# Optimization experiments

Measured on AMD Instinct MI355X. Metric: run time of the kernel, lower is better.

The kernel has to match this reference:

```python
import jax, jax.numpy as jnp
import numpy as np

N_HEADS = 16
HEAD_DIM = 64
STRIDE = 32  # default local_attention_ctx used as stride in 'strided' mode


def _strided_fill_mask(n):
    # Faithful to the torch code: positions where (i >= j) and ((i - j) % stride == 0)
    # get mask value 1, and the code does masked_fill_(mask == 1, -inf),
    # i.e. those positions are set to -inf (inverted polarity, replicated as-is).
    i = jnp.arange(n)[:, None]
    j = jnp.arange(n)[None, :]
    return (i >= j) & (((i - j) % STRIDE) == 0)  # [n, n] bool, True -> -inf


def setup_inputs() -> dict:
    key = jax.random.key(0)
    k_x, k_qkv, k_out = jax.random.split(key, 3)
    b, n, c = 2, 2048, 1024
    inner = N_HEADS * HEAD_DIM  # 1024
    x = jax.random.normal(k_x, (b, n, c), dtype=jnp.float32)
    W_qkv = jax.random.normal(k_qkv, (c, 3 * inner), dtype=jnp.float32) * 0.02
    W_out = jax.random.normal(k_out, (inner, c), dtype=jnp.float32) * 0.02
    b_out = jnp.zeros((c,), dtype=jnp.float32)
    return {"x": x, "W_qkv": W_qkv, "W_out": W_out, "b_out": b_out}


def reference(x, W_qkv, W_out, b_out):
    b, n, c = x.shape
    h, hd = N_HEADS, HEAD_DIM
    scale = c ** (-0.5)  # n_embeddings ** -0.5, as in the original

    qkv = x @ W_qkv                              # [b, n, 3*h*hd]
    q, k, v = jnp.split(qkv, 3, axis=-1)
    def to_heads(t):
        return t.reshape(b, n, h, hd).transpose(0, 2, 1, 3)  # [b, h, n, hd]
    q, k, v = to_heads(q), to_heads(k), to_heads(v)

    dots = jnp.einsum('bhid,bhjd->bhij', q, k) * scale       # [b, h, n, n]
    fill = _strided_fill_mask(n)                             # [n, n]
    dots = jnp.where(fill[None, None], -jnp.inf, dots)

    attn = jax.nn.softmax(dots, axis=-1)
    out = jnp.einsum('bhij,bhjd->bhid', attn, v)             # [b, h, n, hd]
    out = out.transpose(0, 2, 1, 3).reshape(b, n, h * hd)    # [b, n, inner]
    out = out @ W_out + b_out                                # dropout: eval/identity
    return out
```

## Files before the change

kernel.cpp:

```cpp
#include <hip/hip_runtime.h>

typedef __attribute__((ext_vector_type(8))) short bf16x8;
typedef __attribute__((ext_vector_type(4))) float f32x4;

#if __has_builtin(__builtin_amdgcn_exp2f)
#define EXP2F(x) __builtin_amdgcn_exp2f(x)
#else
extern "C" __device__ float __ocml_native_exp2_f32(float);
#define EXP2F(x) __ocml_native_exp2_f32(x)
#endif

__device__ __forceinline__ ushort f32_to_bf16(float f) {
  union { float f; unsigned u; } x; x.f = f;
  unsigned r = x.u + 0x7fffu + ((x.u >> 16) & 1u);
  return (ushort)(r >> 16);
}

__device__ __forceinline__ void load16_to_lds(const void* g, void* l) {
  __builtin_amdgcn_global_load_lds(
      (const __attribute__((address_space(1))) unsigned int*)(
          reinterpret_cast<uintptr_t>(g)),
      (__attribute__((address_space(3))) unsigned int*)(
          reinterpret_cast<uintptr_t>(l)),
      16, 0, 0);
}

__global__ __launch_bounds__(256) void convert_bf16(
    const float* __restrict__ in, ushort* __restrict__ out, int n8)
{
  int i = blockIdx.x * 256 + threadIdx.x;
  if (i >= n8) return;
  const float4* p = (const float4*)(in + (size_t)i * 8);
  float4 a = p[0], b = p[1];
  union { uint4 v; ushort s[8]; } u;
  u.s[0] = f32_to_bf16(a.x); u.s[1] = f32_to_bf16(a.y);
  u.s[2] = f32_to_bf16(a.z); u.s[3] = f32_to_bf16(a.w);
  u.s[4] = f32_to_bf16(b.x); u.s[5] = f32_to_bf16(b.y);
  u.s[6] = f32_to_bf16(b.z); u.s[7] = f32_to_bf16(b.w);
  *(uint4*)(out + (size_t)i * 8) = u.v;
}

__global__ __launch_bounds__(256) void transpose_w(
    const float* __restrict__ in, ushort* __restrict__ out, int R, int C,
    int qcols, float qscale)
{
  __shared__ ushort tile[32][33];
  int t = threadIdx.x, tx = t & 31, ty = t >> 5;
  int rb = blockIdx.y * 32, cb = blockIdx.x * 32;
  float s = (cb + tx) < qcols ? qscale : 1.0f;
#pragma unroll
  for (int k = 0; k < 4; ++k)
    tile[ty + 8 * k][tx] =
        f32_to_bf16(in[(size_t)(rb + ty + 8 * k) * C + cb + tx] * s);
  __syncthreads();
#pragma unroll
  for (int k = 0; k < 4; ++k)
    out[(size_t)(cb + ty + 8 * k) * R + rb + tx] = tile[tx][ty + 8 * k];
}

template <int MODE, typename TC>
__global__ __launch_bounds__(256) void gemm_bt(
    const ushort* __restrict__ A, const ushort* __restrict__ Bt,
    const float* __restrict__ bias, TC* __restrict__ C,
    ushort* __restrict__ Vt, int M, int N, int K)
{
  __shared__ ushort sA[128 * 32];
  __shared__ ushort sB[128 * 32];

  const int t = threadIdx.x;
  const int lane = t & 63, w = t >> 6;
  const int quad = lane >> 4, l16 = lane & 15;
  const int wr = w >> 1, wc = w & 1;
  const int mbase = blockIdx.y * 128, nbase = blockIdx.x * 128;
  const int lrow = lane >> 2, lchunk = (lane & 3) * 8;

  f32x4 acc[4][4];
#pragma unroll
  for (int i = 0; i < 4; ++i)
#pragma unroll
    for (int j = 0; j < 4; ++j)
      acc[i][j] = (f32x4){0.f, 0.f, 0.f, 0.f};

  for (int kb = 0; kb < K; kb += 32) {
    __syncthreads();
#pragma unroll
    for (int r = 0; r < 2; ++r) {
      int rb = w * 32 + r * 16;
      load16_to_lds(&A[(size_t)(mbase + rb + lrow) * K + kb + lchunk], &sA[rb * 32]);
      load16_to_lds(&Bt[(size_t)(nbase + rb + lrow) * K + kb + lchunk], &sB[rb * 32]);
    }
    __syncthreads();

    bf16x8 af[4], bf[4];
#pragma unroll
    for (int mt = 0; mt < 4; ++mt)
      af[mt] = *(const bf16x8*)&sA[(wr * 64 + mt * 16 + l16) * 32 + quad * 8];
#pragma unroll
    for (int nt = 0; nt < 4; ++nt)
      bf[nt] = *(const bf16x8*)&sB[(wc * 64 + nt * 16 + l16) * 32 + quad * 8];
#pragma unroll
    for (int mt = 0; mt < 4; ++mt)
#pragma unroll
      for (int nt = 0; nt < 4; ++nt)
        acc[mt][nt] = __builtin_amdgcn_mfma_f32_16x16x32_bf16(
            af[mt], bf[nt], acc[mt][nt], 0, 0, 0);
  }

#pragma unroll
  for (int mt = 0; mt < 4; ++mt) {
#pragma unroll
    for (int nt = 0; nt < 4; ++nt) {
      int col = nbase + wc * 64 + nt * 16 + l16;
      if constexpr (MODE == 0) {
        float bv = bias ? bias[col] : 0.f;
#pragma unroll
        for (int ri = 0; ri < 4; ++ri) {
          int row = mbase + wr * 64 + mt * 16 + quad * 4 + ri;
          C[(size_t)row * N + col] = acc[mt][nt][ri] + bv;
        }
      } else {
        if (col < 2048) {
#pragma unroll
          for (int ri = 0; ri < 4; ++ri) {
            int row = mbase + wr * 64 + mt * 16 + quad * 4 + ri;
            C[(size_t)row * 2048 + col] = (TC)f32_to_bf16(acc[mt][nt][ri]);
          }
        } else {
          int hh = (col - 2048) >> 6, dd = (col - 2048) & 63;
#pragma unroll
          for (int ri = 0; ri < 4; ++ri) {
            int row = mbase + wr * 64 + mt * 16 + quad * 4 + ri;
            int bb = row >> 11, nn = row & 2047;
            Vt[((size_t)((bb * 16 + hh) * 64 + dd)) * 2048 + nn] =
                f32_to_bf16(acc[mt][nt][ri]);
          }
        }
      }
    }
  }
}

#define NS 2048

__global__ __launch_bounds__(256) void attn_kernel(
    const ushort* __restrict__ qk, const ushort* __restrict__ vt,
    ushort* __restrict__ attn_out)
{
  __shared__ ushort sK[64 * 64];
  __shared__ ushort sV[64 * 64];
  __shared__ ushort sPt[4][32][72];

  const int t = threadIdx.x;
  const int lane = t & 63, w = t >> 6;
  const int quad = lane >> 4, l16 = lane & 15;
  const int bh = blockIdx.y, b = bh >> 4, h = bh & 15;
  const int qbase = blockIdx.x * 128;
  const int rowK = lane >> 3;
  const int csw = ((lane & 7) ^ rowK) * 8;
  const int swz = (l16 & 7);

  bf16x8 qf[2][2];
#pragma unroll
  for (int is = 0; is < 2; ++is)
#pragma unroll
    for (int c = 0; c < 2; ++c)
      qf[is][c] = *(const bf16x8*)&qk[
          ((size_t)(b * NS + qbase + w * 32 + is * 16 + l16)) * 2048 +
          h * 64 + c * 32 + quad * 8];

  bf16x8 ones;
  { union { bf16x8 v; ushort s[8]; } ou;
#pragma unroll
    for (int i = 0; i < 8; ++i) ou.s[i] = 0x3F80;
    ones = ou.v; }

  unsigned amask[2][4][2];
#pragma unroll
  for (int is = 0; is < 2; ++is)
#pragma unroll
    for (int mt = 0; mt < 4; ++mt)
#pragma unroll
      for (int hf = 0; hf < 2; ++hf) {
        int r0 = hf * 2, r1 = hf * 2 + 1;
        int base = is * 16 + l16 - mt * 16 - quad * 4;
        unsigned m = 0xFFFFFFFFu;
        if (((base - r0) & 31) == 0) m &= 0xFFFF0000u;
        if (((base - r1) & 31) == 0) m &= 0x0000FFFFu;
        amask[is][mt][hf] = m;
      }

  const int ib64 = (qbase + w * 32) >> 6;

  f32x4 oacc[2][4];
#pragma unroll
  for (int is = 0; is < 2; ++is)
#pragma unroll
    for (int dt = 0; dt < 4; ++dt) oacc[is][dt] = (f32x4){0.f, 0.f, 0.f, 0.f};
  f32x4 lsum[2];
  lsum[0] = (f32x4){0.f, 0.f, 0.f, 0.f};
  lsum[1] = (f32x4){0.f, 0.f, 0.f, 0.f};

  for (int kb = 0; kb < NS / 64; ++kb) {
    const int kvbase = kb * 64;
    __syncthreads();
#pragma unroll
    for (int g = 0; g < 2; ++g) {
      int rk = w * 16 + g * 8 + rowK;
      load16_to_lds(&qk[((size_t)(b * NS + kvbase + rk)) * 2048 + 1024 +
                        h * 64 + csw],
                    &sK[(w * 16 + g * 8) * 64]);
      load16_to_lds(&vt[((size_t)(bh * 64 + rk)) * 2048 + kvbase + csw],
                    &sV[(w * 16 + g * 8) * 64]);
    }
    __syncthreads();

    f32x4 st[2][4];
#pragma unroll
    for (int is = 0; is < 2; ++is)
#pragma unroll
      for (int mt = 0; mt < 4; ++mt) st[is][mt] = (f32x4){0.f, 0.f, 0.f, 0.f};
#pragma unroll
    for (int mt = 0; mt < 4; ++mt)
#pragma unroll
      for (int c = 0; c < 2; ++c) {
        bf16x8 kf = *(const bf16x8*)&sK[(mt * 16 + l16) * 64 +
                                        (((c * 4 + quad) ^ swz) * 8)];
        st[0][mt] = __builtin_amdgcn_mfma_f32_16x16x32_bf16(
            kf, qf[0][c], st[0][mt], 0, 0, 0);
        st[1][mt] = __builtin_amdgcn_mfma_f32_16x16x32_bf16(
            kf, qf[1][c], st[1][mt], 0, 0, 0);
      }

    if (kb < ib64) {
#pragma unroll
      for (int is = 0; is < 2; ++is)
#pragma unroll
        for (int mt = 0; mt < 4; ++mt) {
          unsigned pb[4];
#pragma unroll
          for (int ri = 0; ri < 4; ++ri) {
            union { float f; unsigned u; } cv;
            cv.f = EXP2F(st[is][mt][ri]);
            pb[ri] = cv.u + 0x8000u;
          }
          unsigned lo = __builtin_amdgcn_perm(pb[1], pb[0], 0x07060302u) &
                        amask[is][mt][0];
          unsigned hi = __builtin_amdgcn_perm(pb[3], pb[2], 0x07060302u) &
                        amask[is][mt][1];
          *(uint2*)&sPt[w][is * 16 + l16][mt * 16 + quad * 4] =
              make_uint2(lo, hi);
        }
    } else if (kb > ib64) {
#pragma unroll
      for (int is = 0; is < 2; ++is)
#pragma unroll
        for (int mt = 0; mt < 4; ++mt) {
          unsigned pb[4];
#pragma unroll
          for (int ri = 0; ri < 4; ++ri) {
            union { float f; unsigned u; } cv;
            cv.f = EXP2F(st[is][mt][ri]);
            pb[ri] = cv.u + 0x8000u;
          }
          unsigned lo = __builtin_amdgcn_perm(pb[1], pb[0], 0x07060302u);
          unsigned hi = __builtin_amdgcn_perm(pb[3], pb[2], 0x07060302u);
          *(uint2*)&sPt[w][is * 16 + l16][mt * 16 + quad * 4] =
              make_uint2(lo, hi);
        }
    } else {
#pragma unroll
      for (int is = 0; is < 2; ++is) {
        int irow = qbase + w * 32 + is * 16 + l16;
#pragma unroll
        for (int mt = 0; mt < 4; ++mt) {
          unsigned pb[4];
#pragma unroll
          for (int ri = 0; ri < 4; ++ri) {
            int j = kvbase + mt * 16 + quad * 4 + ri;
            float p = EXP2F(st[is][mt][ri]);
            unsigned du = (unsigned)(irow - j);
            if ((du & 0x8000001Fu) == 0u) p = 0.f;
            union { float f; unsigned u; } cv; cv.f = p;
            pb[ri] = cv.u + 0x8000u;
          }
          unsigned lo = __builtin_amdgcn_perm(pb[1], pb[0], 0x07060302u);
          unsigned hi = __builtin_amdgcn_perm(pb[3], pb[2], 0x07060302u);
          *(uint2*)&sPt[w][is * 16 + l16][mt * 16 + quad * 4] =
              make_uint2(lo, hi);
        }
      }
    }

#pragma unroll
    for (int c2 = 0; c2 < 2; ++c2) {
      bf16x8 vf[4];
#pragma unroll
      for (int dt = 0; dt < 4; ++dt)
        vf[dt] = *(const bf16x8*)&sV[(dt * 16 + l16) * 64 +
                                     (((c2 * 4 + quad) ^ swz) * 8)];
#pragma unroll
      for (int is = 0; is < 2; ++is) {
        bf16x8 pf = *(const bf16x8*)&sPt[w][is * 16 + l16][c2 * 32 + quad * 8];
        lsum[is] = __builtin_amdgcn_mfma_f32_16x16x32_bf16(
            pf, ones, lsum[is], 0, 0, 0);
#pragma unroll
        for (int dt = 0; dt < 4; ++dt)
          oacc[is][dt] = __builtin_amdgcn_mfma_f32_16x16x32_bf16(
              pf, vf[dt], oacc[is][dt], 0, 0, 0);
      }
    }
  }

#pragma unroll
  for (int is = 0; is < 2; ++is)
#pragma unroll
    for (int ri = 0; ri < 4; ++ri) {
      float inv = __builtin_amdgcn_rcpf(lsum[is][ri]);
      int ig = qbase + w * 32 + is * 16 + quad * 4 + ri;
#pragma unroll
      for (int dt = 0; dt < 4; ++dt)
        attn_out[(size_t)(b * NS + ig) * 1024 + h * 64 + dt * 16 + l16] =
            f32_to_bf16(oacc[is][dt][ri] * inv);
    }
}

extern "C" void kernel_launch(void* const* d_in, const int* in_sizes, int n_in,
                              void* d_out, int out_size, void* d_ws, size_t ws_size,
                              hipStream_t stream) {
  const float* x    = (const float*)d_in[0];
  const float* Wqkv = (const float*)d_in[1];
  const float* Wout = (const float*)d_in[2];
  const float* bout = (const float*)d_in[3];
  float* out = (float*)d_out;

  ushort* qkbuf = (ushort*)d_ws;
  ushort* Vt    = qkbuf + (size_t)4096 * 2048;
  ushort* xb    = Vt + (size_t)32 * 64 * 2048;
  ushort* wT    = xb + (size_t)4096 * 1024;
  ushort* attnb = xb;

  const float QSCALE = 0.04508422002778011f;

  convert_bf16<<<2048, 256, 0, stream>>>(x, xb, 4096 * 1024 / 8);
  transpose_w<<<dim3(3072 / 32, 1024 / 32), 256, 0, stream>>>(
      Wqkv, wT, 1024, 3072, 1024, QSCALE);
  gemm_bt<1, ushort><<<dim3(3072 / 128, 4096 / 128), 256, 0, stream>>>(
      xb, wT, nullptr, qkbuf, Vt, 4096, 3072, 1024);
  attn_kernel<<<dim3(NS / 128, 32), 256, 0, stream>>>(qkbuf, Vt, attnb);
  transpose_w<<<dim3(1024 / 32, 1024 / 32), 256, 0, stream>>>(
      Wout, wT, 1024, 1024, 0, 1.0f);
  gemm_bt<0, float><<<dim3(1024 / 128, 4096 / 128), 256, 0, stream>>>(
      attnb, wT, bout, out, nullptr, 4096, 1024, 1024);
}
```

Baseline: 204.0 us.

## Double-buffer attention K/V, compute V^T via separate GEMM, fuse prep kernels

The attention loop now double-buffers K and V tiles in LDS. The next tile's global-to-LDS load is issued right after the barrier, so only one barrier per iteration is needed and load latency overlaps with MFMA work. The QKV projection is split into a QK GEMM and a separate GEMM that computes V^T directly as Wv^T·x^T, replacing the scattered transposed stores with ordinary row-major writes in a new [h*64+d][b*2048+n] layout. The x conversion and the Wqkv transpose are merged into a single prep launch. Together these cut launch overhead and uncoalesced stores, at the cost of twice the LDS for K/V and one extra GEMM launch.

```diff
diff --git a/kernel.cpp b/kernel.cpp
--- a/kernel.cpp
+++ b/kernel.cpp
@@ -9,6 +9,9 @@
 extern "C" __device__ float __ocml_native_exp2_f32(float);
 #define EXP2F(x) __ocml_native_exp2_f32(x)
 #endif
+
+#define QSCALE 0.04508422002778011f
+#define NS 2048
 
 __device__ __forceinline__ ushort f32_to_bf16(float f) {
   union { float f; unsigned u; } x; x.f = f;
@@ -25,44 +28,58 @@
       16, 0, 0);
 }
 
-__global__ __launch_bounds__(256) void convert_bf16(
-    const float* __restrict__ in, ushort* __restrict__ out, int n8)
-{
-  int i = blockIdx.x * 256 + threadIdx.x;
-  if (i >= n8) return;
-  const float4* p = (const float4*)(in + (size_t)i * 8);
-  float4 a = p[0], b = p[1];
-  union { uint4 v; ushort s[8]; } u;
-  u.s[0] = f32_to_bf16(a.x); u.s[1] = f32_to_bf16(a.y);
-  u.s[2] = f32_to_bf16(a.z); u.s[3] = f32_to_bf16(a.w);
-  u.s[4] = f32_to_bf16(b.x); u.s[5] = f32_to_bf16(b.y);
-  u.s[6] = f32_to_bf16(b.z); u.s[7] = f32_to_bf16(b.w);
-  *(uint4*)(out + (size_t)i * 8) = u.v;
+__global__ __launch_bounds__(256) void prep(
+    const float* __restrict__ x, const float* __restrict__ Wqkv,
+    ushort* __restrict__ xb, ushort* __restrict__ wqkvT)
+{
+  __shared__ ushort tile[32][33];
+  const int bid = blockIdx.x, t = threadIdx.x;
+  if (bid < 2048) {
+    size_t i = (size_t)bid * 256 + t;
+    const float4* p = (const float4*)(x + i * 8);
+    float4 a = p[0], b = p[1];
+    union { uint4 v; ushort s[8]; } u;
+    u.s[0] = f32_to_bf16(a.x); u.s[1] = f32_to_bf16(a.y);
+    u.s[2] = f32_to_bf16(a.z); u.s[3] = f32_to_bf16(a.w);
+    u.s[4] = f32_to_bf16(b.x); u.s[5] = f32_to_bf16(b.y);
+    u.s[6] = f32_to_bf16(b.z); u.s[7] = f32_to_bf16(b.w);
+    *(uint4*)(xb + i * 8) = u.v;
+  } else {
+    int tb = bid - 2048;
+    int cb = (tb % 96) * 32, rb = (tb / 96) * 32;
+    int tx = t & 31, ty = t >> 5;
+    float s = (cb + tx) < 1024 ? QSCALE : 1.0f;
+#pragma unroll
+    for (int k = 0; k < 4; ++k)
+      tile[ty + 8 * k][tx] =
+          f32_to_bf16(Wqkv[(size_t)(rb + ty + 8 * k) * 3072 + cb + tx] * s);
+    __syncthreads();
+#pragma unroll
+    for (int k = 0; k < 4; ++k)
+      wqkvT[(size_t)(cb + ty + 8 * k) * 1024 + rb + tx] = tile[tx][ty + 8 * k];
+  }
 }
 
 __global__ __launch_bounds__(256) void transpose_w(
-    const float* __restrict__ in, ushort* __restrict__ out, int R, int C,
-    int qcols, float qscale)
+    const float* __restrict__ in, ushort* __restrict__ out, int R, int C)
 {
   __shared__ ushort tile[32][33];
   int t = threadIdx.x, tx = t & 31, ty = t >> 5;
   int rb = blockIdx.y * 32, cb = blockIdx.x * 32;
-  float s = (cb + tx) < qcols ? qscale : 1.0f;
 #pragma unroll
   for (int k = 0; k < 4; ++k)
-    tile[ty + 8 * k][tx] =
-        f32_to_bf16(in[(size_t)(rb + ty + 8 * k) * C + cb + tx] * s);
+    tile[ty + 8 * k][tx] = f32_to_bf16(in[(size_t)(rb + ty + 8 * k) * C + cb + tx]);
   __syncthreads();
 #pragma unroll
   for (int k = 0; k < 4; ++k)
     out[(size_t)(cb + ty + 8 * k) * R + rb + tx] = tile[tx][ty + 8 * k];
 }
 
-template <int MODE, typename TC>
+template <typename TC>
 __global__ __launch_bounds__(256) void gemm_bt(
     const ushort* __restrict__ A, const ushort* __restrict__ Bt,
     const float* __restrict__ bias, TC* __restrict__ C,
-    ushort* __restrict__ Vt, int M, int N, int K)
+    int M, int N, int K)
 {
   __shared__ ushort sA[128 * 32];
   __shared__ ushort sB[128 * 32];
@@ -111,43 +128,41 @@
 #pragma unroll
     for (int nt = 0; nt < 4; ++nt) {
       int col = nbase + wc * 64 + nt * 16 + l16;
-      if constexpr (MODE == 0) {
-        float bv = bias ? bias[col] : 0.f;
-#pragma unroll
-        for (int ri = 0; ri < 4; ++ri) {
-          int row = mbase + wr * 64 + mt * 16 + quad * 4 + ri;
-          C[(size_t)row * N + col] = acc[mt][nt][ri] + bv;
-        }
-      } else {
-        if (col < 2048) {
-#pragma unroll
-          for (int ri = 0; ri < 4; ++ri) {
-            int row = mbase + wr * 64 + mt * 16 + quad * 4 + ri;
-            C[(size_t)row * 2048 + col] = (TC)f32_to_bf16(acc[mt][nt][ri]);
-          }
-        } else {
-          int hh = (col - 2048) >> 6, dd = (col - 2048) & 63;
-#pragma unroll
-          for (int ri = 0; ri < 4; ++ri) {
-            int row = mbase + wr * 64 + mt * 16 + quad * 4 + ri;
-            int bb = row >> 11, nn = row & 2047;
-            Vt[((size_t)((bb * 16 + hh) * 64 + dd)) * 2048 + nn] =
-                f32_to_bf16(acc[mt][nt][ri]);
-          }
-        }
-      }
-    }
-  }
-}
-
-#define NS 2048
+      float bv = bias ? bias[col] : 0.f;
+#pragma unroll
+      for (int ri = 0; ri < 4; ++ri) {
+        int row = mbase + wr * 64 + mt * 16 + quad * 4 + ri;
+        float val = acc[mt][nt][ri] + bv;
+        if constexpr (__is_same(TC, float))
+          C[(size_t)row * N + col] = val;
+        else
+          C[(size_t)row * N + col] = f32_to_bf16(val);
+      }
+    }
+  }
+}
+
+__device__ __forceinline__ void stage_kv(
+    const ushort* __restrict__ qk, const ushort* __restrict__ vt,
+    ushort* sKb, ushort* sVb, int b, int h, int kvbase,
+    int w, int rowK, int csw)
+{
+#pragma unroll
+  for (int g = 0; g < 2; ++g) {
+    int rk = w * 16 + g * 8 + rowK;
+    load16_to_lds(&qk[((size_t)(b * NS + kvbase + rk)) * 2048 + 1024 + h * 64 + csw],
+                  &sKb[(w * 16 + g * 8) * 64]);
+    load16_to_lds(&vt[((size_t)(h * 64 + rk)) * 4096 + b * 2048 + kvbase + csw],
+                  &sVb[(w * 16 + g * 8) * 64]);
+  }
+}
 
 __global__ __launch_bounds__(256) void attn_kernel(
     const ushort* __restrict__ qk, const ushort* __restrict__ vt,
     ushort* __restrict__ attn_out)
 {
-  __shared__ ushort sK[64 * 64];
-  __shared__ ushort sV[64 * 64];
+  __shared__ ushort sK[2][64 * 64];
+  __shared__ ushort sV[2][64 * 64];
   __shared__ ushort sPt[4][32][72];
 
   const int t = threadIdx.x;
@@ -157,7 +172,7 @@
   const int qbase = blockIdx.x * 128;
   const int rowK = lane >> 3;
   const int csw = ((lane & 7) ^ rowK) * 8;
-  const int swz = (l16 & 7);
+  const int swz = l16 & 7;
 
   bf16x8 qf[2][2];
 #pragma unroll
@@ -200,19 +215,17 @@
   lsum[0] = (f32x4){0.f, 0.f, 0.f, 0.f};
   lsum[1] = (f32x4){0.f, 0.f, 0.f, 0.f};
 
+  stage_kv(qk, vt, sK[0], sV[0], b, h, 0, w, rowK, csw);
+
   for (int kb = 0; kb < NS / 64; ++kb) {
+    const int cur = kb & 1;
     const int kvbase = kb * 64;
     __syncthreads();
-#pragma unroll
-    for (int g = 0; g < 2; ++g) {
-      int rk = w * 16 + g * 8 + rowK;
-      load16_to_lds(&qk[((size_t)(b * NS + kvbase + rk)) * 2048 + 1024 +
-                        h * 64 + csw],
-                    &sK[(w * 16 + g * 8) * 64]);
-      load16_to_lds(&vt[((size_t)(bh * 64 + rk)) * 2048 + kvbase + csw],
-                    &sV[(w * 16 + g * 8) * 64]);
-    }
-    __syncthreads();
+    if (kb < NS / 64 - 1)
+      stage_kv(qk, vt, sK[cur ^ 1], sV[cur ^ 1], b, h, kvbase + 64, w, rowK, csw);
+
+    const ushort* K = sK[cur];
+    const ushort* V = sV[cur];
 
     f32x4 st[2][4];
 #pragma unroll
@@ -223,8 +236,8 @@
     for (int mt = 0; mt < 4; ++mt)
 #pragma unroll
       for (int c = 0; c < 2; ++c) {
-        bf16x8 kf = *(const bf16x8*)&sK[(mt * 16 + l16) * 64 +
-                                        (((c * 4 + quad) ^ swz) * 8)];
+        bf16x8 kf = *(const bf16x8*)&K[(mt * 16 + l16) * 64 +
+                                       (((c * 4 + quad) ^ swz) * 8)];
         st[0][mt] = __builtin_amdgcn_mfma_f32_16x16x32_bf16(
             kf, qf[0][c], st[0][mt], 0, 0, 0);
         st[1][mt] = __builtin_amdgcn_mfma_f32_16x16x32_bf16(
@@ -296,8 +309,8 @@
       bf16x8 vf[4];
 #pragma unroll
       for (int dt = 0; dt < 4; ++dt)
-        vf[dt] = *(const bf16x8*)&sV[(dt * 16 + l16) * 64 +
-                                     (((c2 * 4 + quad) ^ swz) * 8)];
+        vf[dt] = *(const bf16x8*)&V[(dt * 16 + l16) * 64 +
+                                    (((c2 * 4 + quad) ^ swz) * 8)];
 #pragma unroll
       for (int is = 0; is < 2; ++is) {
         bf16x8 pf = *(const bf16x8*)&sPt[w][is * 16 + l16][c2 * 32 + quad * 8];
@@ -333,22 +346,20 @@
   const float* bout = (const float*)d_in[3];
   float* out = (float*)d_out;
 
-  ushort* qkbuf = (ushort*)d_ws;
-  ushort* Vt    = qkbuf + (size_t)4096 * 2048;
-  ushort* xb    = Vt + (size_t)32 * 64 * 2048;
-  ushort* wT    = xb + (size_t)4096 * 1024;
+  ushort* qk    = (ushort*)d_ws;
+  ushort* vt    = qk + (size_t)4096 * 2048;
+  ushort* xb    = vt + (size_t)1024 * 4096;
+  ushort* wqkvT = xb + (size_t)4096 * 1024;
   ushort* attnb = xb;
-
-  const float QSCALE = 0.04508422002778011f;
-
-  convert_bf16<<<2048, 256, 0, stream>>>(x, xb, 4096 * 1024 / 8);
-  transpose_w<<<dim3(3072 / 32, 1024 / 32), 256, 0, stream>>>(
-      Wqkv, wT, 1024, 3072, 1024, QSCALE);
-  gemm_bt<1, ushort><<<dim3(3072 / 128, 4096 / 128), 256, 0, stream>>>(
-      xb, wT, nullptr, qkbuf, Vt, 4096, 3072, 1024);
-  attn_kernel<<<dim3(NS / 128, 32), 256, 0, stream>>>(qkbuf, Vt, attnb);
-  transpose_w<<<dim3(1024 / 32, 1024 / 32), 256, 0, stream>>>(
-      Wout, wT, 1024, 1024, 0, 1.0f);
-  gemm_bt<0, float><<<dim3(1024 / 128, 4096 / 128), 256, 0, stream>>>(
-      attnb, wT, bout, out, nullptr, 4096, 1024, 1024);
-}
+  ushort* woutT = wqkvT;
+
+  prep<<<2048 + 3072, 256, 0, stream>>>(x, Wqkv, xb, wqkvT);
+  gemm_bt<ushort><<<dim3(16, 32), 256, 0, stream>>>(
+      xb, wqkvT, nullptr, qk, 4096, 2048, 1024);
+  gemm_bt<ushort><<<dim3(32, 8), 256, 0, stream>>>(
+      wqkvT + (size_t)2048 * 1024, xb, nullptr, vt, 1024, 4096, 1024);
+  transpose_w<<<dim3(32, 32), 256, 0, stream>>>(Wout, woutT, 1024, 1024);
+  attn_kernel<<<dim3(NS / 128, 32), 256, 0, stream>>>(qk, vt, attnb);
+  gemm_bt<float><<<dim3(8, 32), 256, 0, stream>>>(
+      attnb, woutT, bout, out, 4096, 1024, 1024);
+}
```

New measurement: 221.3 us. +8.4%, slower.
